# Optimization experiments

Measured on AMD Instinct MI355X. Metric: run time of the kernel, lower is better.

## Reference

```python
import jax, jax.numpy as jnp
import numpy as np


def _rbf_kernel(X, Z, variance, lengthscale):
    # K[n, r] = variance * exp(-||x_n - z_r||^2 / (2 * lengthscale^2))
    x2 = jnp.sum(X * X, axis=-1)[:, None]          # [N, 1]
    z2 = jnp.sum(Z * Z, axis=-1)[None, :]          # [1, R]
    sq = x2 + z2 - 2.0 * (X @ Z.T)                 # [N, R]
    sq = jnp.maximum(sq, 0.0)
    return variance * jnp.exp(-0.5 * sq / (lengthscale * lengthscale))


def setup_inputs() -> dict:
    key = jax.random.key(0)
    ks = jax.random.split(key, 6)
    N, D, S, F, R = 16384, 8, 8, 1024, 2048
    X_star = jax.random.normal(ks[0], (N, D), dtype=jnp.float32)
    ref_points = jax.random.normal(ks[1], (R, D), dtype=jnp.float32)
    omega = jax.random.normal(ks[2], (S, D, F), dtype=jnp.float32)
    two_pi = 2.0 * np.pi
    phase = jax.random.uniform(ks[3], (S, F), dtype=jnp.float32) * two_pi
    feature_weights = jax.random.normal(ks[4], (S, F), dtype=jnp.float32)
    correction_weights = jax.random.normal(ks[5], (S, R), dtype=jnp.float32)
    variance = jnp.ones((), dtype=jnp.float32)
    lengthscale = jnp.ones((), dtype=jnp.float32)
    return {
        "X_star": X_star,
        "ref_points": ref_points,
        "omega": omega,
        "phase": phase,
        "feature_weights": feature_weights,
        "correction_weights": correction_weights,
        "variance": variance,
        "lengthscale": lengthscale,
    }


def reference(X_star, ref_points, omega, phase, feature_weights,
              correction_weights, variance, lengthscale):
    F = omega.shape[-1]
    # RFF prior paths: angles [S, N, F]
    angles = jnp.einsum('nd,sdf->snf', X_star, omega) / lengthscale + phase[:, None, :]
    scale = jnp.sqrt(2.0 * variance / F)
    features = scale * jnp.cos(angles)                       # [S, N, F]
    prior = jnp.sum(features * feature_weights[:, None, :], axis=-1)  # [S, N]
    # Kernel correction term
    K_cross = _rbf_kernel(X_star, ref_points, variance, lengthscale)  # [N, R]
    update = jnp.einsum('nr,sr->sn', K_cross, correction_weights)     # [S, N]
    # mean_fn is None -> zero mean
    mean = jnp.zeros(X_star.shape[0], dtype=X_star.dtype)
    return prior + update + mean[None, :]
```

## Files before the change

### kernel.cpp

```cpp
#include <hip/hip_runtime.h>
#include <math.h>

#ifndef __has_builtin
#define __has_builtin(x) 0
#endif

typedef __attribute__((ext_vector_type(8))) short bf16x8;
typedef __attribute__((ext_vector_type(4))) float f32x4;

__device__ __forceinline__ float fast_fract(float x) {
#if __has_builtin(__builtin_amdgcn_fractf)
    return __builtin_amdgcn_fractf(x);
#else
    return x - floorf(x);
#endif
}
__device__ __forceinline__ float fast_cos2pi(float x) {
#if __has_builtin(__builtin_amdgcn_cosf)
    return __builtin_amdgcn_cosf(x);
#else
    return cosf(x * 6.28318530717958647692f);
#endif
}
__device__ __forceinline__ float fast_exp2(float x) {
#if __has_builtin(__builtin_amdgcn_exp2f)
    return __builtin_amdgcn_exp2f(x);
#else
    return exp2f(x);
#endif
}
__device__ __forceinline__ unsigned short f2bf(float f) {
    unsigned u = __float_as_uint(f);
    return (unsigned short)((u + 0x7FFFu + ((u >> 16) & 1u)) >> 16);
}
__device__ __forceinline__ float bf2f(unsigned short b) {
    return __uint_as_float(((unsigned)b) << 16);
}

constexpr int kN = 16384, kD = 8, kS = 8, kF = 1024, kR = 2048;
constexpr float kInv2Pi = 0.15915494309189535f;
constexpr float kLog2e  = 1.4426950408889634f;
constexpr size_t kWsNeed = (size_t)(512 + 128) * 64 * 16;

__global__ __launch_bounds__(256)
void prep_kernel(const float* __restrict__ omega, const float* __restrict__ phase,
                 const float* __restrict__ Z, const float* __restrict__ lsp,
                 uint4* __restrict__ ws)
{
    const int job  = blockIdx.x * 256 + threadIdx.x;
    const int lane = job & 63;
    const int tile = job >> 6;
    const int g = lane >> 4, c = lane & 15;

    const float inv_ls = 1.0f / lsp[0];
    const float m_ang  = kInv2Pi * inv_ls;
    const float L      = kLog2e * inv_ls * inv_ls;

    unsigned short h[8];
    if (tile < 512) {
        const int s = tile >> 6, ft = tile & 63, f = ft * 16 + c;
        const float* om = omega + s * (kD * kF);
        const float* ph = phase + s * kF;
        #pragma unroll
        for (int j = 0; j < 8; ++j) {
            const int k = g * 8 + j;
            unsigned short v = 0;
            if (k < 16) {
                const int d = k & 7;
                v = f2bf(om[d * kF + f] * m_ang);
            } else if (k < 24) {
                const int d = k - 16;
                const float w = om[d * kF + f] * m_ang;
                v = f2bf(w - bf2f(f2bf(w)));
            } else if (k == 24) {
                v = f2bf(ph[f] * kInv2Pi);
            } else if (k == 25) {
                const float p = ph[f] * kInv2Pi;
                v = f2bf(p - bf2f(f2bf(p)));
            }
            h[j] = v;
        }
    } else {
        const int rt = tile - 512, r = rt * 16 + c;
        const float* zr = Z + r * kD;
        float zz = 0.f;
        #pragma unroll
        for (int d = 0; d < kD; ++d) zz = fmaf(zr[d], zr[d], zz);
        const float zt = -0.5f * L * zz;
        #pragma unroll
        for (int j = 0; j < 8; ++j) {
            const int k = g * 8 + j;
            unsigned short v = 0;
            if (k < 16) {
                v = f2bf(L * zr[k & 7]);
            } else if (k < 24) {
                const float w = L * zr[k - 16];
                v = f2bf(w - bf2f(f2bf(w)));
            } else if (k == 24) {
                v = f2bf(zt);
            } else if (k == 25) {
                v = f2bf(zt - bf2f(f2bf(zt)));
            } else if (k < 28) {
                v = 0x3F80;
            }
            h[j] = v;
        }
    }
    uint4 w;
    w.x = (unsigned)h[0] | ((unsigned)h[1] << 16);
    w.y = (unsigned)h[2] | ((unsigned)h[3] << 16);
    w.z = (unsigned)h[4] | ((unsigned)h[5] << 16);
    w.w = (unsigned)h[6] | ((unsigned)h[7] << 16);
    ws[tile * 64 + lane] = w;
}

__global__ __launch_bounds__(256)
void prior_mfma(const float* __restrict__ X, const float* __restrict__ fw,
                const float* __restrict__ varp, const uint4* __restrict__ wsP,
                float* __restrict__ out)
{
    const int tid  = threadIdx.x;
    const int lane = tid & 63;
    const int wave = __builtin_amdgcn_readfirstlane(tid >> 6);
    const int s  = blockIdx.x & 7;
    const int ng = blockIdx.x >> 3;
    const int ntile = ng * 4 + wave, n0 = ntile * 16;
    const int c = lane & 15, g = lane >> 4;

    float xv[kD];
    {
        const float4 x0 = *reinterpret_cast<const float4*>(X + (n0 + c) * kD);
        const float4 x1 = *reinterpret_cast<const float4*>(X + (n0 + c) * kD + 4);
        xv[0]=x0.x; xv[1]=x0.y; xv[2]=x0.z; xv[3]=x0.w;
        xv[4]=x1.x; xv[5]=x1.y; xv[6]=x1.z; xv[7]=x1.w;
    }
    bf16x8 af;
    if (g == 3) {
        #pragma unroll
        for (int j = 0; j < 8; ++j) af[j] = 0;
        af[0] = (short)0x3F80; af[1] = (short)0x3F80;
    } else if (g == 1) {
        #pragma unroll
        for (int j = 0; j < 8; ++j)
            af[j] = (short)f2bf(xv[j] - bf2f(f2bf(xv[j])));
    } else {
        #pragma unroll
        for (int j = 0; j < 8; ++j) af[j] = (short)f2bf(xv[j]);
    }

    const float scale = sqrtf(2.0f * varp[0] / (float)kF);
    const uint4* bp = wsP + (s * 64) * 64 + lane;
    const float* fwp = fw + s * kF + c;

    float a0 = 0.f, a1 = 0.f, a2 = 0.f, a3 = 0.f;
    #pragma unroll 2
    for (int ft = 0; ft < 64; ++ft) {
        const uint4 bw  = bp[ft * 64];
        const float fwv = fwp[ft * 16];
        const f32x4 dv = __builtin_amdgcn_mfma_f32_16x16x32_bf16(
            af, __builtin_bit_cast(bf16x8, bw), (f32x4){0.f, 0.f, 0.f, 0.f}, 0, 0, 0);
        a0 = fmaf(fwv, fast_cos2pi(fast_fract(dv[0])), a0);
        a1 = fmaf(fwv, fast_cos2pi(fast_fract(dv[1])), a1);
        a2 = fmaf(fwv, fast_cos2pi(fast_fract(dv[2])), a2);
        a3 = fmaf(fwv, fast_cos2pi(fast_fract(dv[3])), a3);
    }
    #pragma unroll
    for (int m = 1; m <= 8; m <<= 1) {
        a0 += __shfl_xor(a0, m); a1 += __shfl_xor(a1, m);
        a2 += __shfl_xor(a2, m); a3 += __shfl_xor(a3, m);
    }
    if (c == 0) {
        float* o = out + s * kN + n0 + g * 4;
        o[0] = scale * a0; o[1] = scale * a1; o[2] = scale * a2; o[3] = scale * a3;
    }
}

__global__ __launch_bounds__(256)
void update_mfma(const float* __restrict__ X, const float* __restrict__ cw,
                 const float* __restrict__ varp, const float* __restrict__ lsp,
                 const uint4* __restrict__ wsU, float* __restrict__ out)
{
    const int tid  = threadIdx.x;
    const int lane = tid & 63;
    const int q = __builtin_amdgcn_readfirstlane(tid >> 6);
    const int n0 = blockIdx.x * 16;
    const int c = lane & 15, g = lane >> 4;

    const float inv_ls = 1.0f / lsp[0];
    const float L = kLog2e * inv_ls * inv_ls;

    float xv[kD];
    {
        const float4 x0 = *reinterpret_cast<const float4*>(X + (n0 + c) * kD);
        const float4 x1 = *reinterpret_cast<const float4*>(X + (n0 + c) * kD + 4);
        xv[0]=x0.x; xv[1]=x0.y; xv[2]=x0.z; xv[3]=x0.w;
        xv[4]=x1.x; xv[5]=x1.y; xv[6]=x1.z; xv[7]=x1.w;
    }
    bf16x8 af;
    if (g == 3) {
        float xx = 0.f;
        #pragma unroll
        for (int d = 0; d < kD; ++d) xx = fmaf(xv[d], xv[d], xx);
        const float xt = -0.5f * L * xx;
        const unsigned short th = f2bf(xt);
        const unsigned short tl = f2bf(xt - bf2f(th));
        #pragma unroll
        for (int j = 0; j < 8; ++j) af[j] = 0;
        af[0] = (short)0x3F80; af[1] = (short)0x3F80;
        af[2] = (short)th;     af[3] = (short)tl;
    } else if (g == 1) {
        #pragma unroll
        for (int j = 0; j < 8; ++j)
            af[j] = (short)f2bf(xv[j] - bf2f(f2bf(xv[j])));
    } else {
        #pragma unroll
        for (int j = 0; j < 8; ++j) af[j] = (short)f2bf(xv[j]);
    }

    float acc[kS][4];
    #pragma unroll
    for (int s2 = 0; s2 < kS; ++s2)
        #pragma unroll
        for (int r = 0; r < 4; ++r) acc[s2][r] = 0.f;

    const uint4* bp = wsU + lane;
    const float* cwp = cw + c;
    const int rt0 = q * 32;
    for (int rt = rt0; rt < rt0 + 32; ++rt) {
        const uint4 bw = bp[rt * 64];
        const f32x4 dv = __builtin_amdgcn_mfma_f32_16x16x32_bf16(
            af, __builtin_bit_cast(bf16x8, bw), (f32x4){0.f, 0.f, 0.f, 0.f}, 0, 0, 0);
        float K[4];
        #pragma unroll
        for (int r = 0; r < 4; ++r) K[r] = fast_exp2(fminf(dv[r], 0.f));
        const int rb = rt * 16;
        #pragma unroll
        for (int s2 = 0; s2 < kS; ++s2) {
            const float cwv = cwp[s2 * kR + rb];
            #pragma unroll
            for (int r = 0; r < 4; ++r) acc[s2][r] = fmaf(K[r], cwv, acc[s2][r]);
        }
    }
    #pragma unroll
    for (int m = 1; m <= 8; m <<= 1)
        #pragma unroll
        for (int s2 = 0; s2 < kS; ++s2)
            #pragma unroll
            for (int r = 0; r < 4; ++r) acc[s2][r] += __shfl_xor(acc[s2][r], m);

    if (c == 0) {
        const float var = varp[0];
        #pragma unroll
        for (int s2 = 0; s2 < kS; ++s2) {
            float* o = out + s2 * kN + n0 + g * 4;
            #pragma unroll
            for (int r = 0; r < 4; ++r) atomicAdd(o + r, var * acc[s2][r]);
        }
    }
}

__global__ __launch_bounds__(512, 8)
void prior_fb(const float* __restrict__ X, const float* __restrict__ omega,
              const float* __restrict__ phase, const float* __restrict__ fw,
              const float* __restrict__ varp, const float* __restrict__ lsp,
              float* __restrict__ out)
{
    const int tid  = threadIdx.x;
    const int nloc = tid & 63;
    const int wave = __builtin_amdgcn_readfirstlane(tid >> 6);
    const int s    = blockIdx.y;
    const int n    = blockIdx.x * 64 + nloc;
    const float variance = varp[0];
    const float inv_ls   = 1.0f / lsp[0];
    const float scale = sqrtf(2.0f * variance / (float)kF);
    float xa[kD];
    {
        const float4 x0 = *reinterpret_cast<const float4*>(X + n * kD);
        const float4 x1 = *reinterpret_cast<const float4*>(X + n * kD + 4);
        const float m = inv_ls * kInv2Pi;
        xa[0]=x0.x*m; xa[1]=x0.y*m; xa[2]=x0.z*m; xa[3]=x0.w*m;
        xa[4]=x1.x*m; xa[5]=x1.y*m; xa[6]=x1.z*m; xa[7]=x1.w*m;
    }
    const float* om  = omega + s * (kD * kF);
    const float* ph  = phase + s * kF;
    const float* fwp = fw    + s * kF;
    const int f0 = wave * 128;
    float acc0 = 0.f, acc1 = 0.f;
    for (int fb = f0; fb < f0 + 128; fb += 8) {
        float cv[8];
        #pragma unroll
        for (int j = 0; j < 8; ++j) {
            float t = ph[fb + j] * kInv2Pi;
            #pragma unroll
            for (int d = 0; d < kD; ++d) t = fmaf(xa[d], om[d * kF + fb + j], t);
            cv[j] = fast_cos2pi(fast_fract(t));
        }
        #pragma unroll
        for (int j = 0; j < 8; j += 2) {
            acc0 = fmaf(fwp[fb + j], cv[j], acc0);
            acc1 = fmaf(fwp[fb + j + 1], cv[j + 1], acc1);
        }
    }
    __shared__ float red[8][64];
    red[wave][nloc] = acc0 + acc1;
    __syncthreads();
    if (tid < 64) {
        float t = 0.f;
        #pragma unroll
        for (int k = 0; k < 8; ++k) t += red[k][tid];
        out[s * kN + blockIdx.x * 64 + tid] = scale * t;
    }
}

__global__ __launch_bounds__(1024, 8)
void update_fb(const float* __restrict__ X, const float* __restrict__ Z,
               const float* __restrict__ cw, const float* __restrict__ varp,
               const float* __restrict__ lsp, float* __restrict__ out)
{
    const int tid  = threadIdx.x;
    const int nloc = tid & 63;
    const int wave = __builtin_amdgcn_readfirstlane(tid >> 6);
    const int n    = blockIdx.x * 64 + nloc;
    const float variance = varp[0];
    const float inv_ls   = 1.0f / lsp[0];
    const float L = kLog2e * inv_ls * inv_ls;
    __shared__ float zt_lds[kR];
    __shared__ float red[16][64][kS + 1];
    float x[kD];
    {
        const float4 x0 = *reinterpret_cast<const float4*>(X + n * kD);
        const float4 x1 = *reinterpret_cast<const float4*>(X + n * kD + 4);
        x[0]=x0.x; x[1]=x0.y; x[2]=x0.z; x[3]=x0.w;
        x[4]=x1.x; x[5]=x1.y; x[6]=x1.z; x[7]=x1.w;
    }
    for (int r = tid; r < kR; r += 1024) {
        const float4 z0 = *reinterpret_cast<const float4*>(Z + r * kD);
        const float4 z1 = *reinterpret_cast<const float4*>(Z + r * kD + 4);
        float z2 = z0.x*z0.x + z0.y*z0.y + z0.z*z0.z + z0.w*z0.w
                 + z1.x*z1.x + z1.y*z1.y + z1.z*z1.z + z1.w*z1.w;
        zt_lds[r] = -0.5f * L * z2;
    }
    __syncthreads();
    float xb[kD]; float x2 = 0.f;
    #pragma unroll
    for (int d = 0; d < kD; ++d) { xb[d] = x[d] * L; x2 = fmaf(x[d], x[d], x2); }
    const float xt = -0.5f * L * x2;
    float accU[2][kS];
    #pragma unroll
    for (int j = 0; j < kS; ++j) { accU[0][j] = 0.f; accU[1][j] = 0.f; }
    const int r0 = wave * 128;
    #pragma unroll 4
    for (int rr = 0; rr < 128; ++rr) {
        const int r = r0 + rr;
        float e = xt + zt_lds[r];
        #pragma unroll
        for (int d = 0; d < kD; ++d) e = fmaf(xb[d], Z[r * kD + d], e);
        e = fminf(e, 0.f);
        const float K = fast_exp2(e);
        #pragma unroll
        for (int j = 0; j < kS; ++j)
            accU[rr & 1][j] = fmaf(K, cw[j * kR + r], accU[rr & 1][j]);
    }
    #pragma unroll
    for (int j = 0; j < kS; ++j) red[wave][nloc][j] = accU[0][j] + accU[1][j];
    __syncthreads();
    if (tid < 512) {
        const int n2 = tid & 63;
        const int jj = tid >> 6;
        float tot = 0.f;
        #pragma unroll
        for (int k = 0; k < 16; ++k) tot += red[k][n2][jj];
        const int idx = jj * kN + blockIdx.x * 64 + n2;
        out[idx] = fmaf(variance, tot, out[idx]);
    }
}

extern "C" void kernel_launch(void* const* d_in, const int* in_sizes, int n_in,
                              void* d_out, int out_size, void* d_ws, size_t ws_size,
                              hipStream_t stream) {
    const float* X  = (const float*)d_in[0];
    const float* Z  = (const float*)d_in[1];
    const float* om = (const float*)d_in[2];
    const float* ph = (const float*)d_in[3];
    const float* fw = (const float*)d_in[4];
    const float* cw = (const float*)d_in[5];
    const float* vp = (const float*)d_in[6];
    const float* lp = (const float*)d_in[7];
    float* out = (float*)d_out;

    if (ws_size >= kWsNeed) {
        uint4* wsP = (uint4*)d_ws;
        uint4* wsU = wsP + (size_t)512 * 64;
        hipLaunchKernelGGL(prep_kernel, dim3(160), dim3(256), 0, stream,
                           om, ph, Z, lp, wsP);
        hipLaunchKernelGGL(prior_mfma, dim3(2048), dim3(256), 0, stream,
                           X, fw, vp, wsP, out);
        hipLaunchKernelGGL(update_mfma, dim3(1024), dim3(256), 0, stream,
                           X, cw, vp, lp, wsU, out);
    } else {
        hipLaunchKernelGGL(prior_fb, dim3(kN / 64, kS), dim3(512), 0, stream,
                           X, om, ph, fw, vp, lp, out);
        hipLaunchKernelGGL(update_fb, dim3(kN / 64), dim3(1024), 0, stream,
                           X, Z, cw, vp, lp, out);
    }
}
```

Measured before the change: 123.0 us.

## Stage MFMA B operands and bf16 correction weights in LDS, double row tiles

The prior kernel now stages the whole per-sample omega/phase B-operand table in shared memory and has each wave handle two 16-row tiles, so each B fragment feeds two MFMAs. The update kernel converts the correction weights to bf16 and transposes them into shared memory, so one 16-byte LDS read supplies all 8 samples in place of 8 strided global loads. It also prefetches the next B fragment. This cuts global memory traffic and load count, but adds a per-block LDS fill and barrier, and bf16 correction weights lose some precision.

```diff
diff --git a/kernel.cpp b/kernel.cpp
--- a/kernel.cpp
+++ b/kernel.cpp
@@ -36,6 +36,8 @@
 __device__ __forceinline__ float bf2f(unsigned short b) {
     return __uint_as_float(((unsigned)b) << 16);
 }
+__device__ __forceinline__ float bf_lo(unsigned u) { return __uint_as_float(u << 16); }
+__device__ __forceinline__ float bf_hi(unsigned u) { return __uint_as_float(u & 0xFFFF0000u); }
 
 constexpr int kN = 16384, kD = 8, kS = 8, kF = 1024, kR = 2048;
 constexpr float kInv2Pi = 0.15915494309189535f;
@@ -114,72 +116,108 @@
     ws[tile * 64 + lane] = w;
 }
 
-__global__ __launch_bounds__(256)
-void prior_mfma(const float* __restrict__ X, const float* __restrict__ fw,
-                const float* __restrict__ varp, const uint4* __restrict__ wsP,
-                float* __restrict__ out)
-{
+__device__ __forceinline__ bf16x8 build_af_x(const float* __restrict__ X,
+                                             int row, int g)
+{
+    float xv[kD];
+    const float4 x0 = *reinterpret_cast<const float4*>(X + row * kD);
+    const float4 x1 = *reinterpret_cast<const float4*>(X + row * kD + 4);
+    xv[0]=x0.x; xv[1]=x0.y; xv[2]=x0.z; xv[3]=x0.w;
+    xv[4]=x1.x; xv[5]=x1.y; xv[6]=x1.z; xv[7]=x1.w;
+    bf16x8 af;
+    if (g == 1) {
+        #pragma unroll
+        for (int j = 0; j < 8; ++j)
+            af[j] = (short)f2bf(xv[j] - bf2f(f2bf(xv[j])));
+    } else {
+        #pragma unroll
+        for (int j = 0; j < 8; ++j) af[j] = (short)f2bf(xv[j]);
+    }
+    return af;
+}
+
+__global__ __launch_bounds__(512, 4)
+void prior_mfma2(const float* __restrict__ X, const float* __restrict__ fw,
+                 const float* __restrict__ varp, const uint4* __restrict__ wsP,
+                 float* __restrict__ out)
+{
+    __shared__ uint4 lds_b[4096];
     const int tid  = threadIdx.x;
     const int lane = tid & 63;
     const int wave = __builtin_amdgcn_readfirstlane(tid >> 6);
-    const int s  = blockIdx.x & 7;
-    const int ng = blockIdx.x >> 3;
-    const int ntile = ng * 4 + wave, n0 = ntile * 16;
+    const int s  = blockIdx.y;
     const int c = lane & 15, g = lane >> 4;
-
-    float xv[kD];
+    const int n0 = blockIdx.x * 256 + wave * 32;
+
     {
-        const float4 x0 = *reinterpret_cast<const float4*>(X + (n0 + c) * kD);
-        const float4 x1 = *reinterpret_cast<const float4*>(X + (n0 + c) * kD + 4);
-        xv[0]=x0.x; xv[1]=x0.y; xv[2]=x0.z; xv[3]=x0.w;
-        xv[4]=x1.x; xv[5]=x1.y; xv[6]=x1.z; xv[7]=x1.w;
-    }
-    bf16x8 af;
+        const uint4* src = wsP + s * 4096;
+        #pragma unroll
+        for (int it = 0; it < 8; ++it)
+            lds_b[it * 512 + tid] = src[it * 512 + tid];
+    }
+
+    bf16x8 af0, af1;
     if (g == 3) {
         #pragma unroll
-        for (int j = 0; j < 8; ++j) af[j] = 0;
-        af[0] = (short)0x3F80; af[1] = (short)0x3F80;
-    } else if (g == 1) {
-        #pragma unroll
-        for (int j = 0; j < 8; ++j)
-            af[j] = (short)f2bf(xv[j] - bf2f(f2bf(xv[j])));
+        for (int j = 0; j < 8; ++j) { af0[j] = 0; af1[j] = 0; }
+        af0[0] = (short)0x3F80; af0[1] = (short)0x3F80;
+        af1[0] = (short)0x3F80; af1[1] = (short)0x3F80;
     } else {
-        #pragma unroll
-        for (int j = 0; j < 8; ++j) af[j] = (short)f2bf(xv[j]);
+        af0 = build_af_x(X, n0 + c, g);
+        af1 = build_af_x(X, n0 + 16 + c, g);
     }
 
     const float scale = sqrtf(2.0f * varp[0] / (float)kF);
-    const uint4* bp = wsP + (s * 64) * 64 + lane;
     const float* fwp = fw + s * kF + c;
 
-    float a0 = 0.f, a1 = 0.f, a2 = 0.f, a3 = 0.f;
+    __syncthreads();
+
+    float acc[2][4];
+    #pragma unroll
+    for (int t = 0; t < 2; ++t)
+        #pragma unroll
+        for (int r = 0; r < 4; ++r) acc[t][r] = 0.f;
+
+    const uint4* lb = lds_b + lane;
     #pragma unroll 2
     for (int ft = 0; ft < 64; ++ft) {
-        const uint4 bw  = bp[ft * 64];
+        const bf16x8 bw = __builtin_bit_cast(bf16x8, lb[ft * 64]);
         const float fwv = fwp[ft * 16];
-        const f32x4 dv = __builtin_amdgcn_mfma_f32_16x16x32_bf16(
-            af, __builtin_bit_cast(bf16x8, bw), (f32x4){0.f, 0.f, 0.f, 0.f}, 0, 0, 0);
-        a0 = fmaf(fwv, fast_cos2pi(fast_fract(dv[0])), a0);
-        a1 = fmaf(fwv, fast_cos2pi(fast_fract(dv[1])), a1);
-        a2 = fmaf(fwv, fast_cos2pi(fast_fract(dv[2])), a2);
-        a3 = fmaf(fwv, fast_cos2pi(fast_fract(dv[3])), a3);
-    }
-    #pragma unroll
-    for (int m = 1; m <= 8; m <<= 1) {
-        a0 += __shfl_xor(a0, m); a1 += __shfl_xor(a1, m);
-        a2 += __shfl_xor(a2, m); a3 += __shfl_xor(a3, m);
-    }
+        const f32x4 d0 = __builtin_amdgcn_mfma_f32_16x16x32_bf16(
+            af0, bw, (f32x4){0.f, 0.f, 0.f, 0.f}, 0, 0, 0);
+        const f32x4 d1 = __builtin_amdgcn_mfma_f32_16x16x32_bf16(
+            af1, bw, (f32x4){0.f, 0.f, 0.f, 0.f}, 0, 0, 0);
+        #pragma unroll
+        for (int r = 0; r < 4; ++r) {
+            acc[0][r] = fmaf(fwv, fast_cos2pi(fast_fract(d0[r])), acc[0][r]);
+            acc[1][r] = fmaf(fwv, fast_cos2pi(fast_fract(d1[r])), acc[1][r]);
+        }
+    }
+
+    #pragma unroll
+    for (int m = 1; m <= 8; m <<= 1)
+        #pragma unroll
+        for (int t = 0; t < 2; ++t)
+            #pragma unroll
+            for (int r = 0; r < 4; ++r)
+                acc[t][r] += __shfl_xor(acc[t][r], m);
+
     if (c == 0) {
-        float* o = out + s * kN + n0 + g * 4;
-        o[0] = scale * a0; o[1] = scale * a1; o[2] = scale * a2; o[3] = scale * a3;
-    }
-}
-
-__global__ __launch_bounds__(256)
-void update_mfma(const float* __restrict__ X, const float* __restrict__ cw,
-                 const float* __restrict__ varp, const float* __restrict__ lsp,
-                 const uint4* __restrict__ wsU, float* __restrict__ out)
-{
+        #pragma unroll
+        for (int t = 0; t < 2; ++t) {
+            float* o = out + s * kN + n0 + t * 16 + g * 4;
+            #pragma unroll
+            for (int r = 0; r < 4; ++r) o[r] = scale * acc[t][r];
+        }
+    }
+}
+
+__global__ __launch_bounds__(256, 4)
+void update_mfma2(const float* __restrict__ X, const float* __restrict__ cw,
+                  const float* __restrict__ varp, const float* __restrict__ lsp,
+                  const uint4* __restrict__ wsU, float* __restrict__ out)
+{
+    __shared__ uint4 cw_lds[2048];
     const int tid  = threadIdx.x;
     const int lane = tid & 63;
     const int q = __builtin_amdgcn_readfirstlane(tid >> 6);
@@ -189,15 +227,25 @@
     const float inv_ls = 1.0f / lsp[0];
     const float L = kLog2e * inv_ls * inv_ls;
 
-    float xv[kD];
     {
+        unsigned short* cwl = reinterpret_cast<unsigned short*>(cw_lds);
+        const float2* cw2 = reinterpret_cast<const float2*>(cw);
+        for (int i = tid; i < kS * kR / 2; i += 256) {
+            const float2 v = cw2[i];
+            const int base = i * 2;
+            const int s2 = base >> 11, r = base & 2047;
+            cwl[r * 8 + s2]       = f2bf(v.x);
+            cwl[(r + 1) * 8 + s2] = f2bf(v.y);
+        }
+    }
+
+    bf16x8 af;
+    if (g == 3) {
+        float xv[kD];
         const float4 x0 = *reinterpret_cast<const float4*>(X + (n0 + c) * kD);
         const float4 x1 = *reinterpret_cast<const float4*>(X + (n0 + c) * kD + 4);
         xv[0]=x0.x; xv[1]=x0.y; xv[2]=x0.z; xv[3]=x0.w;
         xv[4]=x1.x; xv[5]=x1.y; xv[6]=x1.z; xv[7]=x1.w;
-    }
-    bf16x8 af;
-    if (g == 3) {
         float xx = 0.f;
         #pragma unroll
         for (int d = 0; d < kD; ++d) xx = fmaf(xv[d], xv[d], xx);
@@ -208,14 +256,11 @@
         for (int j = 0; j < 8; ++j) af[j] = 0;
         af[0] = (short)0x3F80; af[1] = (short)0x3F80;
         af[2] = (short)th;     af[3] = (short)tl;
-    } else if (g == 1) {
-        #pragma unroll
-        for (int j = 0; j < 8; ++j)
-            af[j] = (short)f2bf(xv[j] - bf2f(f2bf(xv[j])));
     } else {
-        #pragma unroll
-        for (int j = 0; j < 8; ++j) af[j] = (short)f2bf(xv[j]);
-    }
+        af = build_af_x(X, n0 + c, g);
+    }
+
+    __syncthreads();
 
     float acc[kS][4];
     #pragma unroll
@@ -224,29 +269,37 @@
         for (int r = 0; r < 4; ++r) acc[s2][r] = 0.f;
 
     const uint4* bp = wsU + lane;
-    const float* cwp = cw + c;
     const int rt0 = q * 32;
+    uint4 bw = bp[rt0 * 64];
     for (int rt = rt0; rt < rt0 + 32; ++rt) {
-        const uint4 bw = bp[rt * 64];
+        const int nidx = (rt + 1 < rt0 + 32) ? rt + 1 : rt;
+        const uint4 nxt = bp[nidx * 64];
         const f32x4 dv = __builtin_amdgcn_mfma_f32_16x16x32_bf16(
             af, __builtin_bit_cast(bf16x8, bw), (f32x4){0.f, 0.f, 0.f, 0.f}, 0, 0, 0);
         float K[4];
         #pragma unroll
         for (int r = 0; r < 4; ++r) K[r] = fast_exp2(fminf(dv[r], 0.f));
-        const int rb = rt * 16;
-        #pragma unroll
-        for (int s2 = 0; s2 < kS; ++s2) {
-            const float cwv = cwp[s2 * kR + rb];
-            #pragma unroll
-            for (int r = 0; r < 4; ++r) acc[s2][r] = fmaf(K[r], cwv, acc[s2][r]);
-        }
-    }
+        const uint4 cv = cw_lds[rt * 16 + c];
+        float cs[8];
+        cs[0] = bf_lo(cv.x); cs[1] = bf_hi(cv.x);
+        cs[2] = bf_lo(cv.y); cs[3] = bf_hi(cv.y);
+        cs[4] = bf_lo(cv.z); cs[5] = bf_hi(cv.z);
+        cs[6] = bf_lo(cv.w); cs[7] = bf_hi(cv.w);
+        #pragma unroll
+        for (int s2 = 0; s2 < kS; ++s2)
+            #pragma unroll
+            for (int r = 0; r < 4; ++r)
+                acc[s2][r] = fmaf(K[r], cs[s2], acc[s2][r]);
+        bw = nxt;
+    }
+
     #pragma unroll
     for (int m = 1; m <= 8; m <<= 1)
         #pragma unroll
         for (int s2 = 0; s2 < kS; ++s2)
             #pragma unroll
-            for (int r = 0; r < 4; ++r) acc[s2][r] += __shfl_xor(acc[s2][r], m);
+            for (int r = 0; r < 4; ++r)
+                acc[s2][r] += __shfl_xor(acc[s2][r], m);
 
     if (c == 0) {
         const float var = varp[0];
@@ -393,9 +446,9 @@
         uint4* wsU = wsP + (size_t)512 * 64;
         hipLaunchKernelGGL(prep_kernel, dim3(160), dim3(256), 0, stream,
                            om, ph, Z, lp, wsP);
-        hipLaunchKernelGGL(prior_mfma, dim3(2048), dim3(256), 0, stream,
+        hipLaunchKernelGGL(prior_mfma2, dim3(64, 8), dim3(512), 0, stream,
                            X, fw, vp, wsP, out);
-        hipLaunchKernelGGL(update_mfma, dim3(1024), dim3(256), 0, stream,
+        hipLaunchKernelGGL(update_mfma2, dim3(1024), dim3(256), 0, stream,
                            X, cw, vp, lp, wsU, out);
     } else {
         hipLaunchKernelGGL(prior_fb, dim3(kN / 64, kS), dim3(512), 0, stream,
```

Result: slower. 126.3 us (+2.7%).
